# Optimization experiments

Hardware: AMD Instinct MI355X
Metric: run time of the kernel (lower is better)

## Reference

```python
import jax, jax.numpy as jnp
import numpy as np

DIM = 128
NUM_LAYERS = 2
FF_MULT = 4
RADIUS = 0.2
K = 8
B, N, L = 8, 2048, 4096
NEG = -1e30


def setup_inputs() -> dict:
    key = jax.random.key(0)
    ks = jax.random.split(key, 12)
    C = DIM
    s = 1.0 / np.sqrt(C)
    w = lambda k, shape, sc: jax.random.normal(k, shape, dtype=jnp.float32) * sc
    inp = {
        "q_xyz": jax.random.uniform(ks[0], (B, N, 3), dtype=jnp.float32),
        "q_feat": jax.random.normal(ks[1], (B, N, C), dtype=jnp.float32),
        "kv_xyz": jax.random.uniform(ks[2], (B, L, 3), dtype=jnp.float32),
        "kv_feat": jax.random.normal(ks[3], (B, L, C), dtype=jnp.float32),
        "kv_pad": jnp.zeros((B, L), dtype=bool),
        # PointTransformerConv params (stacked over layers)
        "W_lin": w(ks[4], (NUM_LAYERS, C, C), s),   # value projection (with bias)
        "b_lin": jnp.zeros((NUM_LAYERS, C), jnp.float32),
        "W_src": w(ks[5], (NUM_LAYERS, C, C), s),   # lin_src, no bias
        "W_dst": w(ks[6], (NUM_LAYERS, C, C), s),   # lin_dst, no bias
        "W_attn": w(ks[7], (NUM_LAYERS, C, C), s),  # attn_nn = Linear+ReLU
        "b_attn": jnp.zeros((NUM_LAYERS, C), jnp.float32),
        "ln1_g": jnp.ones((NUM_LAYERS, C), jnp.float32),
        "ln1_b": jnp.zeros((NUM_LAYERS, C), jnp.float32),
        "W_ff1": w(ks[8], (NUM_LAYERS, C, FF_MULT * C), s),
        "b_ff1": jnp.zeros((NUM_LAYERS, FF_MULT * C), jnp.float32),
        "W_ff2": w(ks[9], (NUM_LAYERS, FF_MULT * C, C), 1.0 / np.sqrt(FF_MULT * C)),
        "b_ff2": jnp.zeros((NUM_LAYERS, C), jnp.float32),
        "ln2_g": jnp.ones((NUM_LAYERS, C), jnp.float32),
        "ln2_b": jnp.zeros((NUM_LAYERS, C), jnp.float32),
    }
    return inp


def _layernorm(x, g, b):
    mu = x.mean(-1, keepdims=True)
    var = ((x - mu) ** 2).mean(-1, keepdims=True)
    return (x - mu) * jax.lax.rsqrt(var + 1e-5) * g + b


def _gather(feats, idx):
    # feats: [B, L, C], idx: [B, N, K] -> [B, N, K, C]
    b, n, k = idx.shape
    g = jnp.take_along_axis(feats, idx.reshape(b, n * k)[:, :, None], axis=1)
    return g.reshape(b, n, k, feats.shape[-1])


def _forward(q_xyz, q_feat, kv_xyz, kv_feat, kv_pad,
             W_lin, b_lin, W_src, W_dst, W_attn, b_attn,
             ln1_g, ln1_b, W_ff1, b_ff1, W_ff2, b_ff2, ln2_g, ln2_b):
    # radius neighbor search (per-batch, fixed K neighbors with validity mask)
    d2 = jnp.sum((q_xyz[:, :, None, :] - kv_xyz[:, None, :, :]) ** 2, axis=-1)  # [B,N,L]
    valid_pair = (d2 <= RADIUS * RADIUS) & (~kv_pad)[:, None, :]
    negd = jnp.where(valid_pair, -d2, NEG)
    negv, idx = jax.lax.top_k(negd, K)          # [B,N,K] nearest-in-ball
    evalid = negv > 0.5 * NEG                   # edge validity mask [B,N,K]

    out = q_feat
    for i in range(NUM_LAYERS):
        # PointTransformerConv, pos_nn = ZeroPos => delta = 0
        aj = _gather(kv_feat @ W_src[i], idx)                    # [B,N,K,C]
        vj = _gather(kv_feat @ W_lin[i] + b_lin[i], idx)         # [B,N,K,C]
        ai = out @ W_dst[i]                                      # [B,N,C]
        logits = jax.nn.relu((ai[:, :, None, :] - aj) @ W_attn[i] + b_attn[i])
        logits = jnp.where(evalid[..., None], logits, NEG)
        m = logits.max(axis=2, keepdims=True)
        e = jnp.exp(logits - m) * evalid[..., None]
        attn = e / jnp.maximum(e.sum(axis=2, keepdims=True), 1e-9)  # per-channel softmax over neighbors
        upd = jnp.sum(attn * vj, axis=2)                         # [B,N,C] scatter-add over edges
        out = _layernorm(out + upd, ln1_g[i], ln1_b[i])
        h = jax.nn.gelu(out @ W_ff1[i] + b_ff1[i], approximate=False)
        out = _layernorm(out + h @ W_ff2[i] + b_ff2[i], ln2_g[i], ln2_b[i])
    return out


def reference(q_xyz, q_feat, kv_xyz, kv_feat, kv_pad,
              W_lin, b_lin, W_src, W_dst, W_attn, b_attn,
              ln1_g, ln1_b, W_ff1, b_ff1, W_ff2, b_ff2, ln2_g, ln2_b):
    return _forward(q_xyz, q_feat, kv_xyz, kv_feat, kv_pad,
                    W_lin, b_lin, W_src, W_dst, W_attn, b_attn,
                    ln1_g, ln1_b, W_ff1, b_ff1, W_ff2, b_ff2, ln2_g, ln2_b)
```

## Files before the change

kernel.cpp:

```cpp
#include <hip/hip_runtime.h>
#include <hip/hip_bf16.h>
#include <math.h>

#define DIM 128
#define BB 8
#define NN 2048
#define LL 4096
#define KK 8

typedef __hip_bfloat16 bf16;
typedef unsigned long long ull;
typedef __attribute__((ext_vector_type(8))) short short8;
typedef __attribute__((ext_vector_type(4))) float float4v;

__device__ __forceinline__ float toF(float x){ return x; }
__device__ __forceinline__ float toF(bf16 x){ return __bfloat162float(x); }
__device__ __forceinline__ void st(float* p, float v){ *p = v; }
__device__ __forceinline__ void st(bf16*  p, float v){ *p = __float2bfloat16(v); }
__device__ __forceinline__ unsigned short f2bf(float f){
  union { bf16 b; unsigned short u; } cv; cv.b = __float2bfloat16(f); return cv.u;
}

__device__ __forceinline__ float gelu_exact(float x){
  return 0.5f * x * (1.0f + erff(x * 0.70710678118654752f));
}

__device__ __forceinline__ float waveSum64(float v){
  #pragma unroll
  for (int o = 32; o > 0; o >>= 1) v += __shfl_xor(v, o, 64);
  return v;
}
__device__ __forceinline__ float quadSum16(float v){
  #pragma unroll
  for (int o = 8; o > 0; o >>= 1) v += __shfl_xor(v, o, 64);
  return v;
}

__device__ __forceinline__ void topk_insert(float (&bd)[KK], int (&bi)[KK], float d2, int id){
  bd[KK-1] = d2; bi[KK-1] = id;
  #pragma unroll
  for (int s = KK-1; s > 0; --s){
    if (bd[s] < bd[s-1]){
      float td = bd[s]; bd[s] = bd[s-1]; bd[s-1] = td;
      int   ti = bi[s]; bi[s] = bi[s-1]; bi[s-1] = ti;
    }
  }
}
__device__ __forceinline__ void topk_insert_u(ull (&m)[KK], ull key){
  m[KK-1] = key;
  #pragma unroll
  for (int t = KK-1; t > 0; --t){
    if (m[t] < m[t-1]){ ull tmp = m[t]; m[t] = m[t-1]; m[t-1] = tmp; }
  }
}

#define KCHUNK 1024
#define QBLK 8
#define SPL 32
__global__ __launch_bounds__(256) void knn_kernel(const float* __restrict__ q_xyz,
                                                  const float* __restrict__ kv_xyz,
                                                  int* __restrict__ idx)
{
  __shared__ __align__(16) float smem[4112];
  float4* kp = (float4*)smem;
  float*  cd = smem;
  int*    ci = (int*)(smem + 2056);
  const int tid  = threadIdx.x;
  const int s    = tid >> 3;
  const int qloc = tid & 7;
  const int b    = blockIdx.y;
  const int qbase = blockIdx.x * QBLK;
  const size_t qo = ((size_t)b * NN + qbase + qloc) * 3;
  const float qx = q_xyz[qo], qy = q_xyz[qo+1], qz = q_xyz[qo+2];
  const float THR0 = __uint_as_float(0x3D23D70Bu);
  float thr = THR0;
  float bd[KK]; int bi[KK];
  #pragma unroll
  for (int k = 0; k < KK; k++){ bd[k] = 3e38f; bi[k] = -1; }
  const float* kvp = kv_xyz + (size_t)b * LL * 3;
  for (int c0 = 0; c0 < LL; c0 += KCHUNK){
    __syncthreads();
    for (int e = tid; e < KCHUNK; e += 256){
      const size_t o = (size_t)(c0 + e) * 3;
      kp[e] = make_float4(kvp[o], kvp[o+1], kvp[o+2], 0.f);
    }
    __syncthreads();
    #pragma unroll 8
    for (int j = 0; j < KCHUNK/SPL; j++){
      const int e = (j << 5) + s;
      const float4 pnt = kp[e];
      const float dx = qx - pnt.x, dy = qy - pnt.y, dz = qz - pnt.z;
      const float d2 = dx*dx + dy*dy + dz*dz;
      if (d2 < thr){
        topk_insert(bd, bi, d2, c0 + e);
        thr = fminf(bd[KK-1], THR0);
      }
    }
  }
  __syncthreads();
  #pragma unroll
  for (int k = 0; k < KK; k++){
    const int a = qloc*257 + s*8 + k;
    cd[a] = bd[k];
    ci[a] = bi[k];
  }
  __syncthreads();
  if (tid < 64){
    const int q = tid >> 3, g = tid & 7;
    ull m[KK];
    #pragma unroll
    for (int k = 0; k < KK; k++) m[k] = ~0ULL;
    #pragma unroll
    for (int mm = 0; mm < 4; mm++){
      const int sl = g + 8*mm;
      #pragma unroll
      for (int k = 0; k < KK; k++){
        const int a = q*257 + sl*8 + k;
        const ull key = ((ull)__float_as_uint(cd[a]) << 32) | (unsigned)ci[a];
        if (key < m[KK-1]) topk_insert_u(m, key);
      }
    }
    #pragma unroll
    for (int k = 0; k < KK; k++){
      const int a = q*257 + g*8 + k;
      cd[a] = __uint_as_float((unsigned)(m[k] >> 32));
      ci[a] = (int)(unsigned)(m[k] & 0xFFFFFFFFu);
    }
    if (tid < QBLK){
      ull f[KK];
      #pragma unroll
      for (int k = 0; k < KK; k++) f[k] = ~0ULL;
      for (int j = 0; j < 64; j++){
        const int a = tid*257 + j;
        const ull key = ((ull)__float_as_uint(cd[a]) << 32) | (unsigned)ci[a];
        if (key < f[KK-1]) topk_insert_u(f, key);
      }
      const int q = b * NN + qbase + tid;
      #pragma unroll
      for (int k = 0; k < KK; k++) idx[q*KK + k] = (int)(unsigned)(f[k] & 0xFFFFFFFFu);
    }
  }
}

__device__ __forceinline__ void packOne(const float* __restrict__ src,
                                        bf16* __restrict__ dst, int idx, int nshift){
  const int k = idx >> nshift;
  const int n = idx & ((1 << nshift) - 1);
  const int N = 1 << nshift;
  st(&dst[((size_t)(k>>3)*N + n)*8 + (k&7)], src[idx]);
}

__global__ __launch_bounds__(256) void prep_weights(const float* __restrict__ Wlin,
                                                    const float* __restrict__ Wff1,
                                                    const float* __restrict__ Wff2,
                                                    const float* __restrict__ Wsrc,
                                                    const float* __restrict__ Wdst,
                                                    const float* __restrict__ Wattn,
                                                    bf16* __restrict__ WlinP,
                                                    bf16* __restrict__ Wff1P,
                                                    bf16* __restrict__ Wff2P,
                                                    bf16* __restrict__ WsaP,
                                                    bf16* __restrict__ WdaP)
{
  __shared__ float row[2][DIM];
  const int bid = blockIdx.x;
  if (bid < 1152){
    int i = bid*256 + threadIdx.x;
    if (i < 32768){
      const int l = i >> 14, r = i & 16383;
      packOne(Wlin + (size_t)l*16384, WlinP + (size_t)l*16384, r, 7);
    } else if (i < 163840){
      i -= 32768;
      const int l = i >> 16, r = i & 65535;
      packOne(Wff1 + (size_t)l*65536, Wff1P + (size_t)l*65536, r, 9);
    } else if (i < 294912){
      i -= 163840;
      const int l = i >> 16, r = i & 65535;
      packOne(Wff2 + (size_t)l*65536, Wff2P + (size_t)l*65536, r, 7);
    }
  } else {
    const int half = threadIdx.x >> 7;
    const int c = threadIdx.x & 127;
    const int tt = (bid - 1152)*2 + half;
    const int r = tt & 127, which = (tt >> 7) & 1, lay = tt >> 8;
    const float* Wx = (which ? Wdst : Wsrc) + (size_t)lay*DIM*DIM;
    const float* Wa = Wattn + (size_t)lay*DIM*DIM;
    row[half][c] = Wx[r*DIM + c];
    __syncthreads();
    float acc = 0.f;
    for (int j = 0; j < DIM; j++) acc = fmaf(row[half][j], Wa[j*DIM + c], acc);
    bf16* dst = (which ? WdaP : WsaP) + (size_t)lay*DIM*DIM;
    st(&dst[((size_t)(r>>3)*DIM + c)*8 + (r&7)], acc);
  }
}

__device__ __forceinline__ void stage_A_f32(const float* __restrict__ A, size_t r0,
                                            int kd, int kc, unsigned short* As, int tid){
  #pragma unroll
  for (int i = 0; i < 8; i++){
    const int f = tid + i*256;
    const int row = f >> 5, c4 = (f & 31) * 4;
    const float4 v = *(const float4*)&A[(r0+row)*kd + kc + c4];
    uint2 u;
    u.x = (unsigned)f2bf(v.x) | ((unsigned)f2bf(v.y) << 16);
    u.y = (unsigned)f2bf(v.z) | ((unsigned)f2bf(v.w) << 16);
    *(uint2*)&As[row*136 + c4] = u;
  }
}
__device__ __forceinline__ void stage_A_bf16(const bf16* __restrict__ A, size_t r0,
                                             int kd, int kc, unsigned short* As, int tid){
  #pragma unroll
  for (int i = 0; i < 8; i++){
    const int f = tid + i*256;
    const int row = f >> 5, c4 = (f & 31) * 4;
    *(uint2*)&As[row*136 + c4] = *(const uint2*)&A[(r0+row)*kd + kc + c4];
  }
}

template<typename TA, int NDIM, bool GELU>
__global__ __launch_bounds__(256) void mfma_single(const TA* __restrict__ A,
                                                   const bf16* __restrict__ Wp,
                                                   const float* __restrict__ bias,
                                                   bf16* __restrict__ Y)
{
  __shared__ __align__(16) unsigned short As[64*136];
  const int tid = threadIdx.x;
  const size_t r0 = (size_t)blockIdx.x * 64;
  const int nblk = blockIdx.y * 128;
  if (sizeof(TA) == 4) stage_A_f32((const float*)A, r0, 128, 0, As, tid);
  else                 stage_A_bf16((const bf16*)A, r0, 128, 0, As, tid);
  __syncthreads();
  const int wid = tid >> 6, ln = tid & 63, qd = ln >> 4, cl = ln & 15;
  float4v acc[8];
  #pragma unroll
  for (int t = 0; t < 8; t++) acc[t] = (float4v){0.f,0.f,0.f,0.f};
  #pragma unroll
  for (int ks = 0; ks < 4; ks++){
    const short8 a = *(const short8*)&As[(wid*16 + cl)*136 + (ks*4 + qd)*8];
    const short8* wb = (const short8*)Wp + (size_t)(ks*4 + qd)*NDIM + nblk + cl;
    #pragma unroll
    for (int t = 0; t < 8; t++){
      const short8 b = wb[t*16];
      acc[t] = __builtin_amdgcn_mfma_f32_16x16x32_bf16(a, b, acc[t], 0, 0, 0);
    }
  }
  #pragma unroll
  for (int t = 0; t < 8; t++){
    const int col = nblk + t*16 + cl;
    const float bv = bias ? bias[col] : 0.f;
    #pragma unroll
    for (int r = 0; r < 4; r++){
      const size_t row = r0 + wid*16 + qd*4 + r;
      float v = acc[t][r] + bv;
      if (GELU) v = gelu_exact(v);
      st(&Y[row*NDIM + col], v);
    }
  }
}

__global__ __launch_bounds__(256) void mfma_dual_qa(const float* __restrict__ kvf,
                                                    const float* __restrict__ featIn,
                                                    const bf16* __restrict__ Wp0,
                                                    const bf16* __restrict__ Wp1,
                                                    const bf16* __restrict__ WpQ,
                                                    const float* __restrict__ bias1,
                                                    bf16* __restrict__ Y0,
                                                    bf16* __restrict__ Y1,
                                                    bf16* __restrict__ Yq)
{
  __shared__ __align__(16) unsigned short As[64*136];
  const int tid = threadIdx.x;
  const int wid = tid >> 6, ln = tid & 63, qd = ln >> 4, cl = ln & 15;
  if (blockIdx.x < 512){
    const size_t r0 = (size_t)blockIdx.x * 64;
    stage_A_f32(kvf, r0, 128, 0, As, tid);
    __syncthreads();
    float4v ac0[8], ac1[8];
    #pragma unroll
    for (int t = 0; t < 8; t++){ ac0[t] = (float4v){0.f,0.f,0.f,0.f}; ac1[t] = (float4v){0.f,0.f,0.f,0.f}; }
    #pragma unroll
    for (int ks = 0; ks < 4; ks++){
      const short8 a = *(const short8*)&As[(wid*16 + cl)*136 + (ks*4 + qd)*8];
      const size_t wo = (size_t)(ks*4 + qd)*DIM + cl;
      const short8* wb0 = (const short8*)Wp0 + wo;
      const short8* wb1 = (const short8*)Wp1 + wo;
      #pragma unroll
      for (int t = 0; t < 8; t++){
        const short8 b0 = wb0[t*16];
        ac0[t] = __builtin_amdgcn_mfma_f32_16x16x32_bf16(a, b0, ac0[t], 0, 0, 0);
        const short8 b1 = wb1[t*16];
        ac1[t] = __builtin_amdgcn_mfma_f32_16x16x32_bf16(a, b1, ac1[t], 0, 0, 0);
      }
    }
    #pragma unroll
    for (int t = 0; t < 8; t++){
      const int col = t*16 + cl;
      const float bv = bias1[col];
      #pragma unroll
      for (int r = 0; r < 4; r++){
        const size_t row = r0 + wid*16 + qd*4 + r;
        st(&Y0[row*DIM + col], ac0[t][r]);
        st(&Y1[row*DIM + col], ac1[t][r] + bv);
      }
    }
  } else {
    const size_t r0 = (size_t)(blockIdx.x - 512) * 64;
    stage_A_f32(featIn, r0, 128, 0, As, tid);
    __syncthreads();
    float4v acc[8];
    #pragma unroll
    for (int t = 0; t < 8; t++) acc[t] = (float4v){0.f,0.f,0.f,0.f};
    #pragma unroll
    for (int ks = 0; ks < 4; ks++){
      const short8 a = *(const short8*)&As[(wid*16 + cl)*136 + (ks*4 + qd)*8];
      const short8* wb = (const short8*)WpQ + (size_t)(ks*4 + qd)*DIM + cl;
      #pragma unroll
      for (int t = 0; t < 8; t++){
        const short8 b = wb[t*16];
        acc[t] = __builtin_amdgcn_mfma_f32_16x16x32_bf16(a, b, acc[t], 0, 0, 0);
      }
    }
    #pragma unroll
    for (int t = 0; t < 8; t++){
      const int col = t*16 + cl;
      #pragma unroll
      for (int r = 0; r < 4; r++){
        const size_t row = r0 + wid*16 + qd*4 + r;
        st(&Yq[row*DIM + col], acc[t][r]);
      }
    }
  }
}

__global__ __launch_bounds__(256) void mfma_ff2ln(const bf16* __restrict__ A,
                                                  const bf16* __restrict__ Wp,
                                                  const float* __restrict__ b2,
                                                  const bf16* __restrict__ resid,
                                                  const float* __restrict__ g,
                                                  const float* __restrict__ bb,
                                                  float* __restrict__ Y)
{
  __shared__ __align__(16) unsigned short As[64*136];
  const int tid = threadIdx.x;
  const size_t r0 = (size_t)blockIdx.x * 64;
  const int wid = tid >> 6, ln = tid & 63, qd = ln >> 4, cl = ln & 15;
  float4v acc[8];
  #pragma unroll
  for (int t = 0; t < 8; t++) acc[t] = (float4v){0.f,0.f,0.f,0.f};
  for (int kc = 0; kc < 512; kc += 128){
    __syncthreads();
    stage_A_bf16(A, r0, 512, kc, As, tid);
    __syncthreads();
    const int k8c = kc >> 3;
    #pragma unroll
    for (int ks = 0; ks < 4; ks++){
      const short8 a = *(const short8*)&As[(wid*16 + cl)*136 + (ks*4 + qd)*8];
      const short8* wb = (const short8*)Wp + (size_t)(k8c + ks*4 + qd)*DIM + cl;
      #pragma unroll
      for (int t = 0; t < 8; t++){
        const short8 b = wb[t*16];
        acc[t] = __builtin_amdgcn_mfma_f32_16x16x32_bf16(a, b, acc[t], 0, 0, 0);
      }
    }
  }
  float v[8][4];
  #pragma unroll
  for (int t = 0; t < 8; t++){
    const int col = t*16 + cl;
    const float bv = b2[col];
    #pragma unroll
    for (int r = 0; r < 4; r++){
      const size_t row = r0 + wid*16 + qd*4 + r;
      v[t][r] = acc[t][r] + bv + toF(resid[row*DIM + col]);
    }
  }
  #pragma unroll
  for (int r = 0; r < 4; r++){
    float s = 0.f;
    #pragma unroll
    for (int t = 0; t < 8; t++) s += v[t][r];
    const float mu = quadSum16(s) * (1.f/DIM);
    float q = 0.f;
    #pragma unroll
    for (int t = 0; t < 8; t++){ const float d = v[t][r] - mu; q += d*d; }
    const float inv = rsqrtf(quadSum16(q) * (1.f/DIM) + 1e-5f);
    const size_t row = r0 + wid*16 + qd*4 + r;
    #pragma unroll
    for (int t = 0; t < 8; t++){
      const int col = t*16 + cl;
      Y[row*DIM + col] = (v[t][r] - mu) * inv * g[col] + bb[col];
    }
  }
}

__global__ __launch_bounds__(256) void attn_ln1(const bf16* __restrict__ qA,
                                                const bf16* __restrict__ srcA,
                                                const bf16* __restrict__ linp,
                                                const int* __restrict__ idx,
                                                const float* __restrict__ b_attn,
                                                const float* __restrict__ feat,
                                                const float* __restrict__ g,
                                                const float* __restrict__ bb,
                                                bf16* __restrict__ out1)
{
  const int tid = threadIdx.x;
  const int wv = tid >> 6, ln = tid & 63;
  const int q = blockIdx.x * 4 + wv;
  const int b = q >> 11;
  const bf16* sbase = srcA + (size_t)b * LL * DIM;
  const bf16* vbase = linp + (size_t)b * LL * DIM;
  const int c0 = ln, c1 = ln + 64;
  const float qa0 = toF(qA[(size_t)q*DIM + c0]) + b_attn[c0];
  const float qa1 = toF(qA[(size_t)q*DIM + c1]) + b_attn[c1];
  int ids[KK]; float l0[KK], l1[KK];
  float m0 = -1e30f, m1 = -1e30f;
  #pragma unroll
  for (int k = 0; k < KK; k++){
    const int id = idx[q*KK + k]; ids[k] = id;
    if (id >= 0){
      const float s0 = toF(sbase[(size_t)id*DIM + c0]);
      const float s1 = toF(sbase[(size_t)id*DIM + c1]);
      l0[k] = fmaxf(qa0 - s0, 0.f); m0 = fmaxf(m0, l0[k]);
      l1[k] = fmaxf(qa1 - s1, 0.f); m1 = fmaxf(m1, l1[k]);
    } else { l0[k] = 0.f; l1[k] = 0.f; }
  }
  float sum0 = 0.f, sum1 = 0.f, upd0 = 0.f, upd1 = 0.f;
  #pragma unroll
  for (int k = 0; k < KK; k++) if (ids[k] >= 0){
    const float e0 = expf(l0[k] - m0); l0[k] = e0; sum0 += e0;
    const float e1 = expf(l1[k] - m1); l1[k] = e1; sum1 += e1;
  }
  if (sum0 > 0.f){
    const float i0 = 1.f / sum0, i1 = 1.f / sum1;
    #pragma unroll
    for (int k = 0; k < KK; k++) if (ids[k] >= 0){
      upd0 = fmaf(l0[k]*i0, toF(vbase[(size_t)ids[k]*DIM + c0]), upd0);
      upd1 = fmaf(l1[k]*i1, toF(vbase[(size_t)ids[k]*DIM + c1]), upd1);
    }
  }
  const float x0 = feat[(size_t)q*DIM + c0] + upd0;
  const float x1 = feat[(size_t)q*DIM + c1] + upd1;
  const float mu = waveSum64(x0 + x1) * (1.f/DIM);
  const float d0 = x0 - mu, d1 = x1 - mu;
  const float var = waveSum64(d0*d0 + d1*d1) * (1.f/DIM);
  const float inv = rsqrtf(var + 1e-5f);
  st(&out1[(size_t)q*DIM + c0], d0 * inv * g[c0] + bb[c0]);
  st(&out1[(size_t)q*DIM + c1], d1 * inv * g[c1] + bb[c1]);
}

extern "C" void kernel_launch(void* const* d_in, const int* in_sizes, int n_in,
                              void* d_out, int out_size, void* d_ws, size_t ws_size,
                              hipStream_t stream)
{
  const float* q_xyz  = (const float*)d_in[0];
  const float* q_feat = (const float*)d_in[1];
  const float* kv_xyz = (const float*)d_in[2];
  const float* kv_feat= (const float*)d_in[3];
  const float* W_lin  = (const float*)d_in[5];
  const float* b_lin  = (const float*)d_in[6];
  const float* W_src  = (const float*)d_in[7];
  const float* W_dst  = (const float*)d_in[8];
  const float* W_attn = (const float*)d_in[9];
  const float* b_attn = (const float*)d_in[10];
  const float* ln1_g  = (const float*)d_in[11];
  const float* ln1_b  = (const float*)d_in[12];
  const float* W_ff1  = (const float*)d_in[13];
  const float* b_ff1  = (const float*)d_in[14];
  const float* W_ff2  = (const float*)d_in[15];
  const float* b_ff2  = (const float*)d_in[16];
  const float* ln2_g  = (const float*)d_in[17];
  const float* ln2_b  = (const float*)d_in[18];
  float* out = (float*)d_out;

  const int MQ  = BB * NN;
  const int MKV = BB * LL;

  char* p = (char*)d_ws;
  int*   idxb  = (int*)p;   p += (size_t)MQ * KK * 4;
  bf16*  WsaP  = (bf16*)p;  p += (size_t)2 * DIM * DIM * 2;
  bf16*  WdaP  = (bf16*)p;  p += (size_t)2 * DIM * DIM * 2;
  bf16*  WlinP = (bf16*)p;  p += (size_t)2 * DIM * DIM * 2;
  bf16*  Wff1P = (bf16*)p;  p += (size_t)2 * DIM * 4*DIM * 2;
  bf16*  Wff2P = (bf16*)p;  p += (size_t)2 * 4*DIM * DIM * 2;
  float* feat  = (float*)p; p += (size_t)MQ * DIM * 4;
  bf16*  out1  = (bf16*)p;  p += (size_t)MQ * DIM * 2;
  bf16*  srcA  = (bf16*)p;  p += (size_t)MKV * DIM * 2;
  bf16*  linp  = (bf16*)p;  p += (size_t)MKV * DIM * 2;
  bf16*  qA    = (bf16*)p;  p += (size_t)MQ * DIM * 2;
  bf16*  hbuf  = srcA;

  knn_kernel<<<dim3(NN/QBLK, BB), 256, 0, stream>>>(q_xyz, kv_xyz, idxb);
  prep_weights<<<1152 + 256, 256, 0, stream>>>(W_lin, W_ff1, W_ff2, W_src, W_dst,
                                               W_attn, WlinP, Wff1P, Wff2P, WsaP, WdaP);

  for (int i = 0; i < 2; i++){
    const size_t w128 = (size_t)i * DIM * DIM;
    const size_t w512 = (size_t)i * DIM * 4*DIM;
    const float* featIn = (i == 0) ? q_feat : feat;

    mfma_dual_qa<<<MKV/64 + MQ/64, 256, 0, stream>>>(kv_feat, featIn,
        WsaP + w128, WlinP + w128, WdaP + w128, b_lin + i*DIM, srcA, linp, qA);
    attn_ln1<<<MQ/4, 256, 0, stream>>>(qA, srcA, linp, idxb, b_attn + i*DIM, featIn,
                                       ln1_g + i*DIM, ln1_b + i*DIM, out1);
    mfma_single<bf16, 512, true><<<dim3(MQ/64, 4), 256, 0, stream>>>(
        out1, Wff1P + w512, b_ff1 + i*4*DIM, hbuf);
    float* ydst = (i == 1) ? out : feat;
    mfma_ff2ln<<<MQ/64, 256, 0, stream>>>(hbuf, Wff2P + w512, b_ff2 + i*DIM, out1,
                                          ln2_g + i*DIM, ln2_b + i*DIM, ydst);
  }
}
```

Baseline: 333.3 us.

## Replace brute-force radius kNN with uniform grid binning and neighbor-cell search

Adds a binning kernel that sorts key points into a 5x5x5 uniform grid (cell size 0.2, matching the radius) per batch, storing each point's original index in the w component. The query kernel then scans only the 3x3x3 neighbouring cells instead of all 4096 points, and keeps (distance, index) packed as 64-bit keys throughout. This cuts the distance work per query to a small fraction of the brute-force scan, at the cost of an extra launch and a single-block-per-batch binning pass with a serial prefix sum. Tie-breaking stays on the original index, so results should match the brute-force version.

```diff
diff --git a/kernel.cpp b/kernel.cpp
--- a/kernel.cpp
+++ b/kernel.cpp
@@ -36,16 +36,6 @@
   return v;
 }
 
-__device__ __forceinline__ void topk_insert(float (&bd)[KK], int (&bi)[KK], float d2, int id){
-  bd[KK-1] = d2; bi[KK-1] = id;
-  #pragma unroll
-  for (int s = KK-1; s > 0; --s){
-    if (bd[s] < bd[s-1]){
-      float td = bd[s]; bd[s] = bd[s-1]; bd[s-1] = td;
-      int   ti = bi[s]; bi[s] = bi[s-1]; bi[s-1] = ti;
-    }
-  }
-}
 __device__ __forceinline__ void topk_insert_u(ull (&m)[KK], ull key){
   m[KK-1] = key;
   #pragma unroll
@@ -54,17 +44,57 @@
   }
 }
 
-#define KCHUNK 1024
+#define NCELL 5
+#define NC3 125
+__global__ __launch_bounds__(1024) void knn_bin(const float* __restrict__ kv_xyz,
+                                                float4* __restrict__ bpts,
+                                                int* __restrict__ offs )
+{
+  __shared__ int cnt[NC3];
+  __shared__ int off[NC3+1];
+  const int b = blockIdx.x;
+  const int tid = threadIdx.x;
+  if (tid < NC3) cnt[tid] = 0;
+  __syncthreads();
+  const float* kvp = kv_xyz + (size_t)b * LL * 3;
+  float px[4], py[4], pz[4]; int pc[4];
+  #pragma unroll
+  for (int i = 0; i < 4; i++){
+    const int e = tid + i*1024;
+    px[i] = kvp[3*e]; py[i] = kvp[3*e+1]; pz[i] = kvp[3*e+2];
+    const int cx = min((int)(px[i]*5.f), 4);
+    const int cy = min((int)(py[i]*5.f), 4);
+    const int cz = min((int)(pz[i]*5.f), 4);
+    pc[i] = (cz*5 + cy)*5 + cx;
+    atomicAdd(&cnt[pc[i]], 1);
+  }
+  __syncthreads();
+  if (tid == 0){
+    int acc = 0;
+    for (int c = 0; c < NC3; c++){ off[c] = acc; acc += cnt[c]; }
+    off[NC3] = acc;
+  }
+  __syncthreads();
+  if (tid < NC3) cnt[tid] = 0;
+  __syncthreads();
+  float4* dst = bpts + (size_t)b * LL;
+  #pragma unroll
+  for (int i = 0; i < 4; i++){
+    const int e = tid + i*1024;
+    const int pos = off[pc[i]] + atomicAdd(&cnt[pc[i]], 1);
+    dst[pos] = make_float4(px[i], py[i], pz[i], __int_as_float(e));
+  }
+  if (tid < NC3 + 1) offs[b*126 + tid] = off[tid];
+}
+
 #define QBLK 8
 #define SPL 32
-__global__ __launch_bounds__(256) void knn_kernel(const float* __restrict__ q_xyz,
-                                                  const float* __restrict__ kv_xyz,
-                                                  int* __restrict__ idx)
-{
-  __shared__ __align__(16) float smem[4112];
-  float4* kp = (float4*)smem;
-  float*  cd = smem;
-  int*    ci = (int*)(smem + 2056);
+__global__ __launch_bounds__(256) void knn_query(const float* __restrict__ q_xyz,
+                                                 const float4* __restrict__ bpts,
+                                                 const int* __restrict__ offs,
+                                                 int* __restrict__ idx)
+{
+  __shared__ ull cd[QBLK*257];
   const int tid  = threadIdx.x;
   const int s    = tid >> 3;
   const int qloc = tid & 7;
@@ -72,67 +102,59 @@
   const int qbase = blockIdx.x * QBLK;
   const size_t qo = ((size_t)b * NN + qbase + qloc) * 3;
   const float qx = q_xyz[qo], qy = q_xyz[qo+1], qz = q_xyz[qo+2];
-  const float THR0 = __uint_as_float(0x3D23D70Bu);
-  float thr = THR0;
-  float bd[KK]; int bi[KK];
-  #pragma unroll
-  for (int k = 0; k < KK; k++){ bd[k] = 3e38f; bi[k] = -1; }
-  const float* kvp = kv_xyz + (size_t)b * LL * 3;
-  for (int c0 = 0; c0 < LL; c0 += KCHUNK){
-    __syncthreads();
-    for (int e = tid; e < KCHUNK; e += 256){
-      const size_t o = (size_t)(c0 + e) * 3;
-      kp[e] = make_float4(kvp[o], kvp[o+1], kvp[o+2], 0.f);
-    }
-    __syncthreads();
-    #pragma unroll 8
-    for (int j = 0; j < KCHUNK/SPL; j++){
-      const int e = (j << 5) + s;
-      const float4 pnt = kp[e];
-      const float dx = qx - pnt.x, dy = qy - pnt.y, dz = qz - pnt.z;
-      const float d2 = dx*dx + dy*dy + dz*dz;
-      if (d2 < thr){
-        topk_insert(bd, bi, d2, c0 + e);
-        thr = fminf(bd[KK-1], THR0);
-      }
-    }
-  }
-  __syncthreads();
-  #pragma unroll
-  for (int k = 0; k < KK; k++){
-    const int a = qloc*257 + s*8 + k;
-    cd[a] = bd[k];
-    ci[a] = bi[k];
-  }
+  const ull THRKEY = ((ull)0x3D23D70Bu << 32);
+  ull kthr = THRKEY;
+  ull m[KK];
+  #pragma unroll
+  for (int k = 0; k < KK; k++) m[k] = ~0ULL;
+  const int qcx = min((int)(qx*5.f), 4);
+  const int qcy = min((int)(qy*5.f), 4);
+  const int qcz = min((int)(qz*5.f), 4);
+  const int* ofb = offs + b*126;
+  const float4* bp = bpts + (size_t)b * LL;
+  const int cx0 = max(qcx-1, 0), cx1 = min(qcx+1, 4);
+  for (int cz = max(qcz-1,0); cz <= min(qcz+1,4); cz++){
+    for (int cy = max(qcy-1,0); cy <= min(qcy+1,4); cy++){
+      const int rowc = (cz*5 + cy)*5;
+      const int pstart = ofb[rowc + cx0];
+      const int pend   = ofb[rowc + cx1 + 1];
+      for (int p = pstart + s; p < pend; p += SPL){
+        const float4 pt = bp[p];
+        const float dx = qx - pt.x, dy = qy - pt.y, dz = qz - pt.z;
+        const float d2 = dx*dx + dy*dy + dz*dz;
+        const ull key = ((ull)__float_as_uint(d2) << 32) | (unsigned)__float_as_int(pt.w);
+        if (key < kthr){
+          topk_insert_u(m, key);
+          kthr = (m[KK-1] < THRKEY) ? m[KK-1] : THRKEY;
+        }
+      }
+    }
+  }
+  #pragma unroll
+  for (int k = 0; k < KK; k++) cd[qloc*257 + s*8 + k] = m[k];
   __syncthreads();
   if (tid < 64){
     const int q = tid >> 3, g = tid & 7;
-    ull m[KK];
-    #pragma unroll
-    for (int k = 0; k < KK; k++) m[k] = ~0ULL;
-    #pragma unroll
-    for (int mm = 0; mm < 4; mm++){
-      const int sl = g + 8*mm;
+    ull mm[KK];
+    #pragma unroll
+    for (int k = 0; k < KK; k++) mm[k] = ~0ULL;
+    #pragma unroll
+    for (int u = 0; u < 4; u++){
+      const int sl = g + 8*u;
       #pragma unroll
       for (int k = 0; k < KK; k++){
-        const int a = q*257 + sl*8 + k;
-        const ull key = ((ull)__float_as_uint(cd[a]) << 32) | (unsigned)ci[a];
-        if (key < m[KK-1]) topk_insert_u(m, key);
-      }
-    }
-    #pragma unroll
-    for (int k = 0; k < KK; k++){
-      const int a = q*257 + g*8 + k;
-      cd[a] = __uint_as_float((unsigned)(m[k] >> 32));
-      ci[a] = (int)(unsigned)(m[k] & 0xFFFFFFFFu);
-    }
+        const ull key = cd[q*257 + sl*8 + k];
+        if (key < mm[KK-1]) topk_insert_u(mm, key);
+      }
+    }
+    #pragma unroll
+    for (int k = 0; k < KK; k++) cd[q*257 + g*8 + k] = mm[k];
     if (tid < QBLK){
       ull f[KK];
       #pragma unroll
       for (int k = 0; k < KK; k++) f[k] = ~0ULL;
       for (int j = 0; j < 64; j++){
-        const int a = tid*257 + j;
-        const ull key = ((ull)__float_as_uint(cd[a]) << 32) | (unsigned)ci[a];
+        const ull key = cd[tid*257 + j];
         if (key < f[KK-1]) topk_insert_u(f, key);
       }
       const int q = b * NN + qbase + tid;
@@ -476,7 +498,9 @@
   const int MKV = BB * LL;
 
   char* p = (char*)d_ws;
-  int*   idxb  = (int*)p;   p += (size_t)MQ * KK * 4;
+  int*    idxb  = (int*)p;    p += (size_t)MQ * KK * 4;
+  float4* bpts  = (float4*)p; p += (size_t)BB * LL * 16;
+  int*    boffs = (int*)p;    p += (size_t)BB * 126 * 4;
   bf16*  WsaP  = (bf16*)p;  p += (size_t)2 * DIM * DIM * 2;
   bf16*  WdaP  = (bf16*)p;  p += (size_t)2 * DIM * DIM * 2;
   bf16*  WlinP = (bf16*)p;  p += (size_t)2 * DIM * DIM * 2;
@@ -489,7 +513,8 @@
   bf16*  qA    = (bf16*)p;  p += (size_t)MQ * DIM * 2;
   bf16*  hbuf  = srcA;
 
-  knn_kernel<<<dim3(NN/QBLK, BB), 256, 0, stream>>>(q_xyz, kv_xyz, idxb);
+  knn_bin<<<BB, 1024, 0, stream>>>(kv_xyz, bpts, boffs);
+  knn_query<<<dim3(NN/QBLK, BB), 256, 0, stream>>>(q_xyz, bpts, boffs, idxb);
   prep_weights<<<1152 + 256, 256, 0, stream>>>(W_lin, W_ff1, W_ff2, W_src, W_dst,
                                                W_attn, WlinP, Wff1P, Wff2P, WsaP, WdaP);
 
```

Result: faster. 302.6 us (-9.2%).
